# Kernel tuning notes

Hardware: AMD Instinct MI355X
Metric: run time of the kernel (lower is better)

Reference implementation:

```python
import jax, jax.numpy as jnp
import numpy as np

B, S, D = 8, 4096, 1024


def setup_inputs() -> dict:
    key = jax.random.key(0)
    k1, k2, k3, k4 = jax.random.split(key, 4)
    x0 = jax.random.normal(k1, (B, S, D), dtype=jnp.float32)
    x1 = jax.random.normal(k2, (B, S, D), dtype=jnp.float32)
    # skipping prob per (example, timestep)
    skipping_probs = jax.random.uniform(k3, (B, S), dtype=jnp.float32) * 0.5
    # bernoulli noise sampled once in setup (torch samples noise.bernoulli_(probs));
    # keep = 1 - noise, precomputed here so the reference is deterministic.
    keep = (jax.random.uniform(k4, (B, S)) >= skipping_probs).astype(jnp.int32)
    return {"x0": x0, "x1": x1, "skipping_probs": skipping_probs, "keep": keep}


def _compact(x, keep):
    """Move kept timesteps to the front (stable order), zero-pad the tail.

    Equivalent to torch's per-example nonzero -> index_select -> pad -> stack,
    except the output is padded to the full S instead of the data-dependent
    max kept length (extra columns are exactly the zero padding).
    x: [B, S, D], keep: [B, S] in {0,1} -> [B, S, D]
    """
    # stable argsort: kept (key 0) before skipped (key 1), original order preserved
    order = jnp.argsort(1 - keep, axis=1)          # [B, S]
    gathered = jnp.take_along_axis(x, order[:, :, None], axis=1)  # [B, S, D]
    n_kept = jnp.sum(keep, axis=1, keepdims=True)  # [B, 1]
    valid = jnp.arange(x.shape[1])[None, :] < n_kept  # [B, S]
    return gathered * valid[:, :, None].astype(x.dtype)


def reference(x0, x1, skipping_probs, keep):
    # skipping_probs only feeds the (already-sampled) bernoulli mask `keep`.
    return (_compact(x0, keep), _compact(x1, keep))
```

## Files before the change

kernel.cpp:

```cpp
#include <hip/hip_runtime.h>
#include <hip/hip_bf16.h>


#define BB 8
#define SS 4096
#define DD 1024
#define D4 (DD / 4)

typedef float f4 __attribute__((ext_vector_type(4)));

__global__ __launch_bounds__(1024) void scan_kernel(
    const int* __restrict__ keep,
    int* __restrict__ src_idx,
    int* __restrict__ n_kept)
{
    const int b = blockIdx.x;
    const int t = threadIdx.x;
    __shared__ int wave_sums[16];

    const int* krow = keep + b * SS;
    const int base = t * 4;
    const int k0 = krow[base + 0];
    const int k1 = krow[base + 1];
    const int k2 = krow[base + 2];
    const int k3 = krow[base + 3];
    const int local = k0 + k1 + k2 + k3;

    const int lane = t & 63;
    const int wid  = t >> 6;

    int incl = local;
    #pragma unroll
    for (int off = 1; off < 64; off <<= 1) {
        int v = __shfl_up(incl, off, 64);
        if (lane >= off) incl += v;
    }
    if (lane == 63) wave_sums[wid] = incl;
    __syncthreads();

    if (t < 16) {
        int v = wave_sums[t];
        #pragma unroll
        for (int off = 1; off < 16; off <<= 1) {
            int u = __shfl_up(v, off, 64);
            if (t >= off) v += u;
        }
        wave_sums[t] = v;
    }
    __syncthreads();

    const int wave_off = (wid > 0) ? wave_sums[wid - 1] : 0;
    int d = wave_off + incl - local;

    int* dst = src_idx + b * SS;
    if (k0) dst[d++] = base + 0;
    if (k1) dst[d++] = base + 1;
    if (k2) dst[d++] = base + 2;
    if (k3) dst[d++] = base + 3;

    if (t == 0) n_kept[b] = wave_sums[15];
}

#define COPY_BLOCKS 2048
__global__ __launch_bounds__(256) void compact_copy_kernel(
    const f4* __restrict__ x0,
    const f4* __restrict__ x1,
    const int* __restrict__ src_idx,
    const int* __restrict__ n_kept,
    f4* __restrict__ out0,
    f4* __restrict__ out1)
{
    const int t = threadIdx.x;

    for (int row = blockIdx.x; row < BB * SS; row += COPY_BLOCKS) {
        const int b = row >> 12;
        const int r = row & (SS - 1);
        const int nk = n_kept[b];
        const int dst_off = row * D4 + t;

        if (r < nk) {
            const int s = src_idx[row];
            const int src_off = (b * SS + s) * D4 + t;
            f4 v0 = __builtin_nontemporal_load(&x0[src_off]);
            f4 v1 = __builtin_nontemporal_load(&x1[src_off]);
            __builtin_nontemporal_store(v0, &out0[dst_off]);
            __builtin_nontemporal_store(v1, &out1[dst_off]);
        } else {
            f4 z = {0.f, 0.f, 0.f, 0.f};
            __builtin_nontemporal_store(z, &out0[dst_off]);
            __builtin_nontemporal_store(z, &out1[dst_off]);
        }
    }
}

extern "C" void kernel_launch(void* const* d_in, const int* in_sizes, int n_in,
                              void* d_out, int out_size, void* d_ws, size_t ws_size,
                              hipStream_t stream) {
    const f4* x0  = (const f4*)d_in[0];
    const f4* x1  = (const f4*)d_in[1];
    const int* keep = (const int*)d_in[3];

    float* out = (float*)d_out;
    f4* out0 = (f4*)out;
    f4* out1 = (f4*)(out + (size_t)BB * SS * DD);

    int* src_idx = (int*)d_ws;
    int* n_kept  = src_idx + BB * SS;

    scan_kernel<<<BB, 1024, 0, stream>>>(keep, src_idx, n_kept);
    compact_copy_kernel<<<COPY_BLOCKS, 256, 0, stream>>>(x0, x1, src_idx, n_kept,
                                                         out0, out1);
}
```

Measured before the change: 92.14 us.

## Fuse prefix-scan into compaction copy kernel with per-block redundant scan in LDS

Merges the separate scan kernel and copy kernel into one launch. Each block recomputes the batch row's prefix scan of the keep mask into shared memory and then copies its strided subset of rows. This removes the extra launch, the serialized low-parallelism scan kernel, and the global index round trip, at the cost of redundant keep reads and scan work in every block.

```diff
diff --git a/kernel.cpp b/kernel.cpp
--- a/kernel.cpp
+++ b/kernel.cpp
@@ -6,25 +6,40 @@
 #define SS 4096
 #define DD 1024
 #define D4 (DD / 4)
+#define BPB 256
+#define RPB (SS / BPB)
 
 typedef float f4 __attribute__((ext_vector_type(4)));
 
-__global__ __launch_bounds__(1024) void scan_kernel(
+__global__ __launch_bounds__(256) void fused_compact_kernel(
+    const f4* __restrict__ x0,
+    const f4* __restrict__ x1,
     const int* __restrict__ keep,
-    int* __restrict__ src_idx,
-    int* __restrict__ n_kept)
+    f4* __restrict__ out0,
+    f4* __restrict__ out1)
 {
-    const int b = blockIdx.x;
+    __shared__ int lds_src[SS];
+    __shared__ int wave_sums[4];
+
     const int t = threadIdx.x;
-    __shared__ int wave_sums[16];
+    const int b = blockIdx.x >> 8;
+    const int j = blockIdx.x & (BPB - 1);
 
-    const int* krow = keep + b * SS;
-    const int base = t * 4;
-    const int k0 = krow[base + 0];
-    const int k1 = krow[base + 1];
-    const int k2 = krow[base + 2];
-    const int k3 = krow[base + 3];
-    const int local = k0 + k1 + k2 + k3;
+    const int4* krow4 = (const int4*)(keep + b * SS);
+    int kk[16];
+    {
+        const int4 a0 = krow4[4 * t + 0];
+        const int4 a1 = krow4[4 * t + 1];
+        const int4 a2 = krow4[4 * t + 2];
+        const int4 a3 = krow4[4 * t + 3];
+        kk[0]  = a0.x; kk[1]  = a0.y; kk[2]  = a0.z; kk[3]  = a0.w;
+        kk[4]  = a1.x; kk[5]  = a1.y; kk[6]  = a1.z; kk[7]  = a1.w;
+        kk[8]  = a2.x; kk[9]  = a2.y; kk[10] = a2.z; kk[11] = a2.w;
+        kk[12] = a3.x; kk[13] = a3.y; kk[14] = a3.z; kk[15] = a3.w;
+    }
+    int local = 0;
+    #pragma unroll
+    for (int q = 0; q < 16; ++q) local += kk[q];
 
     const int lane = t & 63;
     const int wid  = t >> 6;
@@ -38,55 +53,36 @@
     if (lane == 63) wave_sums[wid] = incl;
     __syncthreads();
 
-    if (t < 16) {
-        int v = wave_sums[t];
-        #pragma unroll
-        for (int off = 1; off < 16; off <<= 1) {
-            int u = __shfl_up(v, off, 64);
-            if (t >= off) v += u;
-        }
-        wave_sums[t] = v;
+    int wave_off = 0, nk = 0;
+    #pragma unroll
+    for (int w = 0; w < 4; ++w) {
+        const int v = wave_sums[w];
+        if (w < wid) wave_off += v;
+        nk += v;
+    }
+
+    int d = wave_off + incl - local;
+    const int base_s = t * 16;
+    #pragma unroll
+    for (int q = 0; q < 16; ++q) {
+        if (kk[q]) lds_src[d++] = base_s + q;
     }
     __syncthreads();
 
-    const int wave_off = (wid > 0) ? wave_sums[wid - 1] : 0;
-    int d = wave_off + incl - local;
+    const int batch_base = b * SS * D4 + t;
 
-    int* dst = src_idx + b * SS;
-    if (k0) dst[d++] = base + 0;
-    if (k1) dst[d++] = base + 1;
-    if (k2) dst[d++] = base + 2;
-    if (k3) dst[d++] = base + 3;
-
-    if (t == 0) n_kept[b] = wave_sums[15];
-}
-
-#define COPY_BLOCKS 2048
-__global__ __launch_bounds__(256) void compact_copy_kernel(
-    const f4* __restrict__ x0,
-    const f4* __restrict__ x1,
-    const int* __restrict__ src_idx,
-    const int* __restrict__ n_kept,
-    f4* __restrict__ out0,
-    f4* __restrict__ out1)
-{
-    const int t = threadIdx.x;
-
-    for (int row = blockIdx.x; row < BB * SS; row += COPY_BLOCKS) {
-        const int b = row >> 12;
-        const int r = row & (SS - 1);
-        const int nk = n_kept[b];
-        const int dst_off = row * D4 + t;
-
+    for (int i = 0; i < RPB; ++i) {
+        const int r = j + (i << 8);
+        const int dst_off = batch_base + r * D4;
         if (r < nk) {
-            const int s = src_idx[row];
-            const int src_off = (b * SS + s) * D4 + t;
+            const int s = lds_src[r];
+            const int src_off = batch_base + s * D4;
             f4 v0 = __builtin_nontemporal_load(&x0[src_off]);
             f4 v1 = __builtin_nontemporal_load(&x1[src_off]);
             __builtin_nontemporal_store(v0, &out0[dst_off]);
             __builtin_nontemporal_store(v1, &out1[dst_off]);
         } else {
-            f4 z = {0.f, 0.f, 0.f, 0.f};
+            const f4 z = {0.f, 0.f, 0.f, 0.f};
             __builtin_nontemporal_store(z, &out0[dst_off]);
             __builtin_nontemporal_store(z, &out1[dst_off]);
         }
@@ -104,10 +100,5 @@
     f4* out0 = (f4*)out;
     f4* out1 = (f4*)(out + (size_t)BB * SS * DD);
 
-    int* src_idx = (int*)d_ws;
-    int* n_kept  = src_idx + BB * SS;
-
-    scan_kernel<<<BB, 1024, 0, stream>>>(keep, src_idx, n_kept);
-    compact_copy_kernel<<<COPY_BLOCKS, 256, 0, stream>>>(x0, x1, src_idx, n_kept,
-                                                         out0, out1);
+    fused_compact_kernel<<<BB * BPB, 256, 0, stream>>>(x0, x1, keep, out0, out1);
 }
```

After: 88.61 us. 3.8% less time.
